# Kernel optimization log

Hardware: AMD Instinct MI355X
Metric: run time of the kernel (lower is better)

Reference implementation:

```python
import jax, jax.numpy as jnp
import numpy as np

N_NODES = 50000
N_EDGES = 800000
D = 96        # node_dim
DE = 96       # edge_dim
K_HOPS = 4
K = 2         # module's k; uses edge_attr[:, k-1]


def setup_inputs() -> dict:
    key = jax.random.key(0)
    ks = jax.random.split(key, 12)
    s = 1.0 / np.sqrt(D)
    se = 1.0 / np.sqrt(DE)
    s2 = 1.0 / np.sqrt(2 * D)
    return {
        "V": jax.random.normal(ks[0], (N_NODES, D), jnp.float32),
        "V_in": jax.random.normal(ks[1], (N_NODES, D), jnp.float32),
        "E": jax.random.normal(ks[2], (N_EDGES, DE), jnp.float32),
        "edge_attr": jax.random.uniform(ks[3], (N_EDGES, K_HOPS), jnp.float32),
        "src": jax.random.randint(ks[4], (N_EDGES,), 0, N_NODES),
        "dst": jax.random.randint(ks[5], (N_EDGES,), 0, N_NODES),
        # NodePooling linear A: node_dim -> node_dim
        "A_w": jax.random.uniform(ks[6], (D, D), jnp.float32, -s, s),
        "A_b": jax.random.uniform(ks[7], (D,), jnp.float32, -s, s),
        # M: edge_dim -> node_dim
        "M_w": jax.random.uniform(ks[8], (DE, D), jnp.float32, -se, se),
        "M_b": jax.random.uniform(ks[9], (D,), jnp.float32, -se, se),
        # W: 2*node_dim -> node_dim
        "W_w": jax.random.uniform(ks[10], (2 * D, D), jnp.float32, -s2, s2),
        "W_b": jax.random.uniform(ks[11], (D,), jnp.float32, -s2, s2),
    }


def reference(V, V_in, E, edge_attr, src, dst, A_w, A_b, M_w, M_b, W_w, W_b):
    # V = LeakyReLU(V, 0.2)
    V = jax.nn.leaky_relu(V, negative_slope=0.2)
    # NodePooling: ReLU(Linear(V))
    Vp = jax.nn.relu(V @ A_w + A_b)                      # [N, D]
    # edge projection
    Ep = E @ M_w + M_b                                   # [M, D]
    khop = edge_attr[:, K - 1:K]                         # [M, 1]
    # message: (src['V'] + data['E']) * KHOP, then sum-aggregate to dst
    msg = (Vp[src] + Ep) * khop                          # [M, D]
    agg = jax.ops.segment_sum(msg, dst, num_segments=N_NODES)  # [N, D]
    # cat aggregate with V_in, project, relu
    out = jax.nn.relu(jnp.concatenate([agg, V_in], axis=-1) @ W_w + W_b)
    return out
```

## Files before the change

### kernel.cpp

```cpp
#include <hip/hip_runtime.h>
#include <hip/hip_bf16.h>

#define NN 50000
#define NE 800000
#define DD 96
#define SVP 100
#define CAP 64

typedef float f4 __attribute__((ext_vector_type(4)));
typedef int   i4 __attribute__((ext_vector_type(4)));

__global__ __launch_bounds__(256) void k_vp(
    const float* __restrict__ V, const float* __restrict__ Aw,
    const float* __restrict__ Ab, float* __restrict__ Vp,
    int* __restrict__ cnt)
{
    __shared__ float sW[DD * DD];
    __shared__ float sV[64 * SVP];
    __shared__ float sB[DD];

    const int tid = threadIdx.x;
    const int gt = blockIdx.x * 256 + tid;
    if (gt < NN) cnt[gt] = 0;

    for (int i = tid; i < DD * DD / 4; i += 256)
        reinterpret_cast<f4*>(sW)[i] = reinterpret_cast<const f4*>(Aw)[i];
    if (tid < DD / 4)
        reinterpret_cast<f4*>(sB)[tid] = reinterpret_cast<const f4*>(Ab)[tid];

    const int row0 = blockIdx.x * 64;
    const int nr = min(64, NN - row0);
    for (int i = tid; i < nr * (DD / 4); i += 256) {
        const int r = i / (DD / 4);
        const int c = i % (DD / 4);
        f4 v = reinterpret_cast<const f4*>(V + (size_t)(row0 + r) * DD)[c];
        v[0] = v[0] > 0.f ? v[0] : 0.2f * v[0];
        v[1] = v[1] > 0.f ? v[1] : 0.2f * v[1];
        v[2] = v[2] > 0.f ? v[2] : 0.2f * v[2];
        v[3] = v[3] > 0.f ? v[3] : 0.2f * v[3];
        reinterpret_cast<f4*>(sV + r * SVP)[c] = v;
    }
    __syncthreads();

    const int cg = tid & 15;
    const int rg = tid >> 4;
    const int c0 = cg * 6;
    const int r0 = rg * 4;

    float acc[4][6];
#pragma unroll
    for (int rr = 0; rr < 4; ++rr)
#pragma unroll
        for (int j = 0; j < 6; ++j) acc[rr][j] = sB[c0 + j];

#pragma unroll 4
    for (int k = 0; k < DD; ++k) {
        float x[4];
#pragma unroll
        for (int rr = 0; rr < 4; ++rr) x[rr] = sV[(r0 + rr) * SVP + k];
#pragma unroll
        for (int j = 0; j < 6; ++j) {
            const float w = sW[k * DD + c0 + j];
#pragma unroll
            for (int rr = 0; rr < 4; ++rr)
                acc[rr][j] = fmaf(x[rr], w, acc[rr][j]);
        }
    }

#pragma unroll
    for (int rr = 0; rr < 4; ++rr) {
        const int row = row0 + r0 + rr;
        if (row < NN) {
#pragma unroll
            for (int j = 0; j < 6; ++j)
                Vp[(size_t)row * DD + c0 + j] = fmaxf(acc[rr][j], 0.f);
        }
    }
}

__global__ __launch_bounds__(256) void k_scatter(
    const int* __restrict__ src, const int* __restrict__ dst,
    const float* __restrict__ ea, int* __restrict__ cnt,
    i4* __restrict__ aux)
{
    const int e = blockIdx.x * 256 + threadIdx.x;
    if (e >= NE) return;
    const int d = dst[e];
    const int pos = atomicAdd(&cnt[d], 1);
    i4 a;
    a.x = src[e];
    a.y = e;
    a.z = __float_as_int(ea[(size_t)e * 4 + 1]);
    a.w = 0;
    if (pos < CAP)
        __builtin_nontemporal_store(a, aux + (size_t)d * CAP + pos);
}

__global__ __launch_bounds__(256, 4) void k_aggout(
    const float* __restrict__ Vp, const float* __restrict__ E,
    const int* __restrict__ cnt, const i4* __restrict__ aux,
    const float* __restrict__ Vin, const float* __restrict__ Mw,
    const float* __restrict__ Mb, const float* __restrict__ Ww,
    const float* __restrict__ Wb, float* __restrict__ out)
{
    __shared__ float sAgg[32 * SVP];
    __shared__ float sG[32 * SVP];
    __shared__ float sW[32 * DD];
    __shared__ float sB[DD];
    __shared__ float sS[32];

    const int tid = threadIdx.x;
    const int row0 = blockIdx.x * 32;

    {
        const int grp = tid >> 5;
        const int gl = tid & 31;
        const bool act = (gl < 24);

        i4 apre[4];
        int n[4];
#pragma unroll
        for (int i = 0; i < 4; ++i) {
            const int node = row0 + grp * 4 + i;
            const bool ok = (node < NN);
            apre[i] = ok ? __builtin_nontemporal_load(aux + (size_t)node * CAP + gl)
                         : i4{0, 0, 0, 0};
            n[i] = ok ? min(cnt[node], CAP) : 0;
        }

#pragma unroll
        for (int i = 0; i < 4; ++i) {
            const int nl = grp * 4 + i;
            const int node = row0 + nl;
            if (node >= NN) break;

            f4 av = {0.f, 0.f, 0.f, 0.f};
            f4 ag = {0.f, 0.f, 0.f, 0.f};
            float wsum = 0.f;

            i4 a = apre[i];
            const int nfirst = min(n[i], 32);

            int j = 0;
            for (; j + 8 <= nfirst; j += 8) {
                int ss[8], ee[8];
                float ww[8];
#pragma unroll
                for (int q = 0; q < 8; ++q) {
                    ss[q] = __shfl(a.x, j + q, 32);
                    ee[q] = __shfl(a.y, j + q, 32);
                    ww[q] = __shfl(__int_as_float(a.z), j + q, 32);
                }
                f4 Ev[8], Vv[8];
#pragma unroll
                for (int q = 0; q < 8; ++q) {
                    if (act) {
                        Ev[q] = __builtin_nontemporal_load(
                            reinterpret_cast<const f4*>(E + (size_t)ee[q] * DD) + gl);
                        Vv[q] = *(reinterpret_cast<const f4*>(Vp + (size_t)ss[q] * DD) + gl);
                    } else {
                        Ev[q] = f4{0, 0, 0, 0};
                        Vv[q] = f4{0, 0, 0, 0};
                    }
                }
#pragma unroll
                for (int q = 0; q < 8; ++q) {
#pragma unroll
                    for (int c = 0; c < 4; ++c) {
                        av[c] = fmaf(ww[q], Vv[q][c], av[c]);
                        ag[c] = fmaf(ww[q], Ev[q][c], ag[c]);
                    }
                    wsum += ww[q];
                }
            }
            for (; j + 4 <= nfirst; j += 4) {
                int ss[4], ee[4];
                float ww[4];
#pragma unroll
                for (int q = 0; q < 4; ++q) {
                    ss[q] = __shfl(a.x, j + q, 32);
                    ee[q] = __shfl(a.y, j + q, 32);
                    ww[q] = __shfl(__int_as_float(a.z), j + q, 32);
                }
                f4 Ev[4], Vv[4];
#pragma unroll
                for (int q = 0; q < 4; ++q) {
                    if (act) {
                        Ev[q] = __builtin_nontemporal_load(
                            reinterpret_cast<const f4*>(E + (size_t)ee[q] * DD) + gl);
                        Vv[q] = *(reinterpret_cast<const f4*>(Vp + (size_t)ss[q] * DD) + gl);
                    } else {
                        Ev[q] = f4{0, 0, 0, 0};
                        Vv[q] = f4{0, 0, 0, 0};
                    }
                }
#pragma unroll
                for (int q = 0; q < 4; ++q) {
#pragma unroll
                    for (int c = 0; c < 4; ++c) {
                        av[c] = fmaf(ww[q], Vv[q][c], av[c]);
                        ag[c] = fmaf(ww[q], Ev[q][c], ag[c]);
                    }
                    wsum += ww[q];
                }
            }
            for (; j < nfirst; ++j) {
                const int s0 = __shfl(a.x, j, 32), e0 = __shfl(a.y, j, 32);
                const float w0 = __shfl(__int_as_float(a.z), j, 32);
                f4 E0 = {0, 0, 0, 0}, V0 = {0, 0, 0, 0};
                if (act) {
                    E0 = __builtin_nontemporal_load(
                        reinterpret_cast<const f4*>(E + (size_t)e0 * DD) + gl);
                    V0 = *(reinterpret_cast<const f4*>(Vp + (size_t)s0 * DD) + gl);
                }
#pragma unroll
                for (int c = 0; c < 4; ++c) {
                    av[c] = fmaf(w0, V0[c], av[c]);
                    ag[c] = fmaf(w0, E0[c], ag[c]);
                }
                wsum += w0;
            }

            if (n[i] > 32) {
                i4 a2 = __builtin_nontemporal_load(
                    aux + (size_t)node * CAP + 32 + gl);
                const int rem = n[i] - 32;
                for (int jj = 0; jj < rem; ++jj) {
                    const int s0 = __shfl(a2.x, jj, 32), e0 = __shfl(a2.y, jj, 32);
                    const float w0 = __shfl(__int_as_float(a2.z), jj, 32);
                    f4 E0 = {0, 0, 0, 0}, V0 = {0, 0, 0, 0};
                    if (act) {
                        E0 = __builtin_nontemporal_load(
                            reinterpret_cast<const f4*>(E + (size_t)e0 * DD) + gl);
                        V0 = *(reinterpret_cast<const f4*>(Vp + (size_t)s0 * DD) + gl);
                    }
#pragma unroll
                    for (int c = 0; c < 4; ++c) {
                        av[c] = fmaf(w0, V0[c], av[c]);
                        ag[c] = fmaf(w0, E0[c], ag[c]);
                    }
                    wsum += w0;
                }
            }

            if (act) {
                *reinterpret_cast<f4*>(sAgg + nl * SVP + gl * 4) = av;
                *reinterpret_cast<f4*>(sG + nl * SVP + gl * 4) = ag;
            }
            if (gl == 0) sS[nl] = wsum;
        }
    }
    __syncthreads();

    const int cg = tid & 15;
    const int rg = tid >> 4;
    const int c0 = cg * 6;
    const int r0 = rg * 2;

    auto loadW = [&](const float* wsrc) {
        for (int i = tid; i < 32 * DD / 4; i += 256)
            reinterpret_cast<f4*>(sW)[i] = reinterpret_cast<const f4*>(wsrc)[i];
    };
    auto loadB = [&](const float* bsrc) {
        if (tid < DD / 4)
            reinterpret_cast<f4*>(sB)[tid] = reinterpret_cast<const f4*>(bsrc)[tid];
    };

    loadW(Mw); loadB(Mb);
    __syncthreads();

    float a[2][6];
#pragma unroll
    for (int rr = 0; rr < 2; ++rr) {
        const float sv = sS[r0 + rr];
#pragma unroll
        for (int j = 0; j < 6; ++j)
            a[rr][j] = sAgg[(r0 + rr) * SVP + c0 + j] + sv * sB[c0 + j];
    }
#pragma unroll
    for (int ch = 0; ch < 3; ++ch) {
        if (ch) {
            __syncthreads();
            loadW(Mw + ch * 32 * DD);
            __syncthreads();
        }
        const int kb = ch * 32;
#pragma unroll 4
        for (int k = 0; k < 32; ++k) {
            const float x0 = sG[r0 * SVP + kb + k];
            const float x1 = sG[(r0 + 1) * SVP + kb + k];
#pragma unroll
            for (int j = 0; j < 6; ++j) {
                const float w = sW[k * DD + c0 + j];
                a[0][j] = fmaf(x0, w, a[0][j]);
                a[1][j] = fmaf(x1, w, a[1][j]);
            }
        }
    }
    __syncthreads();
#pragma unroll
    for (int rr = 0; rr < 2; ++rr)
#pragma unroll
        for (int j = 0; j < 6; ++j)
            sAgg[(r0 + rr) * SVP + c0 + j] = a[rr][j];

    {
        const int nr = min(32, NN - row0);
        __syncthreads();
        for (int i = tid; i < nr * (DD / 4); i += 256) {
            const int r = i / (DD / 4);
            const int c = i % (DD / 4);
            reinterpret_cast<f4*>(sG + r * SVP)[c] =
                reinterpret_cast<const f4*>(Vin + (size_t)(row0 + r) * DD)[c];
        }
    }

    loadW(Ww); loadB(Wb);
    __syncthreads();

    float o[2][6];
#pragma unroll
    for (int rr = 0; rr < 2; ++rr)
#pragma unroll
        for (int j = 0; j < 6; ++j) o[rr][j] = sB[c0 + j];
#pragma unroll
    for (int ch = 0; ch < 3; ++ch) {
        if (ch) {
            __syncthreads();
            loadW(Ww + ch * 32 * DD);
            __syncthreads();
        }
        const int kb = ch * 32;
#pragma unroll 4
        for (int k = 0; k < 32; ++k) {
            const float x0 = sAgg[r0 * SVP + kb + k];
            const float x1 = sAgg[(r0 + 1) * SVP + kb + k];
#pragma unroll
            for (int j = 0; j < 6; ++j) {
                const float w = sW[k * DD + c0 + j];
                o[0][j] = fmaf(x0, w, o[0][j]);
                o[1][j] = fmaf(x1, w, o[1][j]);
            }
        }
    }

#pragma unroll
    for (int ch = 0; ch < 3; ++ch) {
        __syncthreads();
        loadW(Ww + (size_t)(96 + ch * 32) * DD);
        __syncthreads();
        const int kb = ch * 32;
#pragma unroll 4
        for (int k = 0; k < 32; ++k) {
            const float x0 = sG[r0 * SVP + kb + k];
            const float x1 = sG[(r0 + 1) * SVP + kb + k];
#pragma unroll
            for (int j = 0; j < 6; ++j) {
                const float w = sW[k * DD + c0 + j];
                o[0][j] = fmaf(x0, w, o[0][j]);
                o[1][j] = fmaf(x1, w, o[1][j]);
            }
        }
    }

#pragma unroll
    for (int rr = 0; rr < 2; ++rr) {
        const int row = row0 + r0 + rr;
        if (row < NN) {
#pragma unroll
            for (int j = 0; j < 6; ++j)
                out[(size_t)row * DD + c0 + j] = fmaxf(o[rr][j], 0.f);
        }
    }
}

extern "C" void kernel_launch(void* const* d_in, const int* in_sizes, int n_in,
                              void* d_out, int out_size, void* d_ws, size_t ws_size,
                              hipStream_t stream)
{
    const float* V   = (const float*)d_in[0];
    const float* Vin = (const float*)d_in[1];
    const float* E   = (const float*)d_in[2];
    const float* ea  = (const float*)d_in[3];
    const int*   src = (const int*)d_in[4];
    const int*   dst = (const int*)d_in[5];
    const float* Aw  = (const float*)d_in[6];
    const float* Ab  = (const float*)d_in[7];
    const float* Mw  = (const float*)d_in[8];
    const float* Mb  = (const float*)d_in[9];
    const float* Ww  = (const float*)d_in[10];
    const float* Wb  = (const float*)d_in[11];
    float* out = (float*)d_out;

    float* Vp  = (float*)d_ws;
    int*   cnt = (int*)(Vp + (size_t)NN * DD);
    size_t aux_off = (size_t)NN * DD + NN;
    aux_off = (aux_off + 3) & ~(size_t)3;
    i4*    aux = (i4*)((float*)d_ws + aux_off);

    k_vp<<<(NN + 63) / 64, 256, 0, stream>>>(V, Aw, Ab, Vp, cnt);
    k_scatter<<<(NE + 255) / 256, 256, 0, stream>>>(src, dst, ea, cnt, aux);
    k_aggout<<<(NN + 31) / 32, 256, 0, stream>>>(Vp, E, cnt, aux, Vin,
                                                 Mw, Mb, Ww, Wb, out);
}
```

Measured before the change: 226.9 us.

## Pre-stream edge features in scatter kernel to warm cache for aggregation

The scatter kernel now streams the whole E tensor and sums it into a value kept alive by an empty asm, so E lines are pulled into cache before the aggregation kernel gathers them. The E gathers in the aggregation kernel switch from nontemporal to normal loads so they can hit those cached lines. V_in loads and output stores become nontemporal, and the edge_attr read becomes one 16-byte vector load. The cost is a full extra pass over E, which is larger than the last-level cache, so the warmed lines may be evicted before aggregation uses them.

```diff
diff --git a/kernel.cpp b/kernel.cpp
--- a/kernel.cpp
+++ b/kernel.cpp
@@ -81,16 +81,30 @@
 __global__ __launch_bounds__(256) void k_scatter(
     const int* __restrict__ src, const int* __restrict__ dst,
     const float* __restrict__ ea, int* __restrict__ cnt,
-    i4* __restrict__ aux)
+    i4* __restrict__ aux, const float* __restrict__ E)
 {
     const int e = blockIdx.x * 256 + threadIdx.x;
     if (e >= NE) return;
+
+    {
+        const f4* Ef = reinterpret_cast<const f4*>(E);
+        f4 s = {0.f, 0.f, 0.f, 0.f};
+#pragma unroll
+        for (int q = 0; q < 24; ++q) {
+            const f4 t = Ef[(size_t)q * NE + e];
+            s[0] += t[0]; s[1] += t[1]; s[2] += t[2]; s[3] += t[3];
+        }
+        float keep = s[0] + s[1] + s[2] + s[3];
+        asm volatile("" :: "v"(keep));
+    }
+
     const int d = dst[e];
     const int pos = atomicAdd(&cnt[d], 1);
+    const f4 eav = *reinterpret_cast<const f4*>(ea + (size_t)e * 4);
     i4 a;
     a.x = src[e];
     a.y = e;
-    a.z = __float_as_int(ea[(size_t)e * 4 + 1]);
+    a.z = __float_as_int(eav[1]);
     a.w = 0;
     if (pos < CAP)
         __builtin_nontemporal_store(a, aux + (size_t)d * CAP + pos);
@@ -155,8 +169,7 @@
 #pragma unroll
                 for (int q = 0; q < 8; ++q) {
                     if (act) {
-                        Ev[q] = __builtin_nontemporal_load(
-                            reinterpret_cast<const f4*>(E + (size_t)ee[q] * DD) + gl);
+                        Ev[q] = *(reinterpret_cast<const f4*>(E + (size_t)ee[q] * DD) + gl);
                         Vv[q] = *(reinterpret_cast<const f4*>(Vp + (size_t)ss[q] * DD) + gl);
                     } else {
                         Ev[q] = f4{0, 0, 0, 0};
@@ -186,8 +199,7 @@
 #pragma unroll
                 for (int q = 0; q < 4; ++q) {
                     if (act) {
-                        Ev[q] = __builtin_nontemporal_load(
-                            reinterpret_cast<const f4*>(E + (size_t)ee[q] * DD) + gl);
+                        Ev[q] = *(reinterpret_cast<const f4*>(E + (size_t)ee[q] * DD) + gl);
                         Vv[q] = *(reinterpret_cast<const f4*>(Vp + (size_t)ss[q] * DD) + gl);
                     } else {
                         Ev[q] = f4{0, 0, 0, 0};
@@ -209,8 +221,7 @@
                 const float w0 = __shfl(__int_as_float(a.z), j, 32);
                 f4 E0 = {0, 0, 0, 0}, V0 = {0, 0, 0, 0};
                 if (act) {
-                    E0 = __builtin_nontemporal_load(
-                        reinterpret_cast<const f4*>(E + (size_t)e0 * DD) + gl);
+                    E0 = *(reinterpret_cast<const f4*>(E + (size_t)e0 * DD) + gl);
                     V0 = *(reinterpret_cast<const f4*>(Vp + (size_t)s0 * DD) + gl);
                 }
 #pragma unroll
@@ -230,8 +241,7 @@
                     const float w0 = __shfl(__int_as_float(a2.z), jj, 32);
                     f4 E0 = {0, 0, 0, 0}, V0 = {0, 0, 0, 0};
                     if (act) {
-                        E0 = __builtin_nontemporal_load(
-                            reinterpret_cast<const f4*>(E + (size_t)e0 * DD) + gl);
+                        E0 = *(reinterpret_cast<const f4*>(E + (size_t)e0 * DD) + gl);
                         V0 = *(reinterpret_cast<const f4*>(Vp + (size_t)s0 * DD) + gl);
                     }
 #pragma unroll
@@ -310,8 +320,8 @@
         for (int i = tid; i < nr * (DD / 4); i += 256) {
             const int r = i / (DD / 4);
             const int c = i % (DD / 4);
-            reinterpret_cast<f4*>(sG + r * SVP)[c] =
-                reinterpret_cast<const f4*>(Vin + (size_t)(row0 + r) * DD)[c];
+            reinterpret_cast<f4*>(sG + r * SVP)[c] = __builtin_nontemporal_load(
+                reinterpret_cast<const f4*>(Vin + (size_t)(row0 + r) * DD) + c);
         }
     }
 
@@ -367,9 +377,15 @@
     for (int rr = 0; rr < 2; ++rr) {
         const int row = row0 + r0 + rr;
         if (row < NN) {
-#pragma unroll
-            for (int j = 0; j < 6; ++j)
-                out[(size_t)row * DD + c0 + j] = fmaxf(o[rr][j], 0.f);
+            f4 lo = {fmaxf(o[rr][0], 0.f), fmaxf(o[rr][1], 0.f),
+                     fmaxf(o[rr][2], 0.f), fmaxf(o[rr][3], 0.f)};
+            float* op = out + (size_t)row * DD + c0;
+            __builtin_nontemporal_store(lo[0], op + 0);
+            __builtin_nontemporal_store(lo[1], op + 1);
+            __builtin_nontemporal_store(lo[2], op + 2);
+            __builtin_nontemporal_store(lo[3], op + 3);
+            __builtin_nontemporal_store(fmaxf(o[rr][4], 0.f), op + 4);
+            __builtin_nontemporal_store(fmaxf(o[rr][5], 0.f), op + 5);
         }
     }
 }
@@ -399,7 +415,7 @@
     i4*    aux = (i4*)((float*)d_ws + aux_off);
 
     k_vp<<<(NN + 63) / 64, 256, 0, stream>>>(V, Aw, Ab, Vp, cnt);
-    k_scatter<<<(NE + 255) / 256, 256, 0, stream>>>(src, dst, ea, cnt, aux);
+    k_scatter<<<(NE + 255) / 256, 256, 0, stream>>>(src, dst, ea, cnt, aux, E);
     k_aggout<<<(NN + 31) / 32, 256, 0, stream>>>(Vp, E, cnt, aux, Vin,
                                                  Mw, Mb, Ww, Wb, out);
 }
```

Result: slower. 276.5 us (+21.8%).

## Double-buffer E row gathers into LDS via global_load_lds with wave-per-node aggregation

Applied to the files above, without the earlier changes.

Reworks the gather phase so each 64-lane wave handles 8 nodes in turn. Rows of E are streamed into a per-wave double-buffered LDS stage with direct global-to-LDS loads, and the next chunk is prefetched while the current one is accumulated. Vp rows are still read into registers, split across two half-waves whose partial sums are combined with shuffles. This aims to hide gather latency and use all lanes. In exchange it adds waitcnt/sched_barrier hand-tuning, drops the occupancy hint, and processes nodes serially per wave with less memory-level parallelism across nodes.

```diff
diff --git a/kernel.cpp b/kernel.cpp
--- a/kernel.cpp
+++ b/kernel.cpp
@@ -9,6 +9,8 @@
 
 typedef float f4 __attribute__((ext_vector_type(4)));
 typedef int   i4 __attribute__((ext_vector_type(4)));
+typedef const __attribute__((address_space(1))) float gfloat_t;
+typedef __attribute__((address_space(3))) float lfloat_t;
 
 __global__ __launch_bounds__(256) void k_vp(
     const float* __restrict__ V, const float* __restrict__ Aw,
@@ -96,7 +98,7 @@
         __builtin_nontemporal_store(a, aux + (size_t)d * CAP + pos);
 }
 
-__global__ __launch_bounds__(256, 4) void k_aggout(
+__global__ __launch_bounds__(256) void k_aggout(
     const float* __restrict__ Vp, const float* __restrict__ E,
     const int* __restrict__ cnt, const i4* __restrict__ aux,
     const float* __restrict__ Vin, const float* __restrict__ Mw,
@@ -105,153 +107,124 @@
 {
     __shared__ float sAgg[32 * SVP];
     __shared__ float sG[32 * SVP];
-    __shared__ float sW[32 * DD];
+    __shared__ float sStage[4 * 2 * 768];
     __shared__ float sB[DD];
     __shared__ float sS[32];
 
     const int tid = threadIdx.x;
+    const int lane = tid & 63;
+    const int wid = tid >> 6;
     const int row0 = blockIdx.x * 32;
 
     {
-        const int grp = tid >> 5;
-        const int gl = tid & 31;
-        const bool act = (gl < 24);
-
-        i4 apre[4];
-        int n[4];
-#pragma unroll
-        for (int i = 0; i < 4; ++i) {
-            const int node = row0 + grp * 4 + i;
-            const bool ok = (node < NN);
-            apre[i] = ok ? __builtin_nontemporal_load(aux + (size_t)node * CAP + gl)
-                         : i4{0, 0, 0, 0};
-            n[i] = ok ? min(cnt[node], CAP) : 0;
-        }
-
-#pragma unroll
-        for (int i = 0; i < 4; ++i) {
-            const int nl = grp * 4 + i;
+        const int c4l = lane % 24;
+        const int rsel = (lane >= 24 && lane < 48) ? 1 : 0;
+        const int stgwave = wid * 1536;
+
+        for (int i = 0; i < 8; ++i) {
+            const int nl = wid * 8 + i;
             const int node = row0 + nl;
             if (node >= NN) break;
 
+            const i4 a = __builtin_nontemporal_load(aux + (size_t)node * CAP + lane);
+            const int n = min(cnt[node], CAP);
+
+            if (n == 0) {
+                if (lane < 24) {
+                    f4 z = {0.f, 0.f, 0.f, 0.f};
+                    *reinterpret_cast<f4*>(sAgg + nl * SVP + lane * 4) = z;
+                    *reinterpret_cast<f4*>(sG + nl * SVP + lane * 4) = z;
+                }
+                if (lane == 0) sS[nl] = 0.f;
+                continue;
+            }
+
+            const int nm1 = n - 1;
+            const float wz = __int_as_float(a.z);
+            const int nsc = (n + 7) >> 3;
+
             f4 av = {0.f, 0.f, 0.f, 0.f};
             f4 ag = {0.f, 0.f, 0.f, 0.f};
-            float wsum = 0.f;
-
-            i4 a = apre[i];
-            const int nfirst = min(n[i], 32);
-
-            int j = 0;
-            for (; j + 8 <= nfirst; j += 8) {
-                int ss[8], ee[8];
-                float ww[8];
-#pragma unroll
-                for (int q = 0; q < 8; ++q) {
-                    ss[q] = __shfl(a.x, j + q, 32);
-                    ee[q] = __shfl(a.y, j + q, 32);
-                    ww[q] = __shfl(__int_as_float(a.z), j + q, 32);
-                }
-                f4 Ev[8], Vv[8];
-#pragma unroll
-                for (int q = 0; q < 8; ++q) {
-                    if (act) {
-                        Ev[q] = __builtin_nontemporal_load(
-                            reinterpret_cast<const f4*>(E + (size_t)ee[q] * DD) + gl);
-                        Vv[q] = *(reinterpret_cast<const f4*>(Vp + (size_t)ss[q] * DD) + gl);
-                    } else {
-                        Ev[q] = f4{0, 0, 0, 0};
-                        Vv[q] = f4{0, 0, 0, 0};
+
+            auto STAGE = [&](int sc, int b) {
+                const int base = stgwave + b * 768;
+#pragma unroll
+                for (int k = 0; k < 3; ++k) {
+                    const int m = k * 64 + lane;
+                    const int row = m / 24;
+                    const int col = m - row * 24;
+                    const int gr = min(sc * 8 + row, nm1);
+                    const int eid = __shfl(a.y, gr, 64);
+                    __builtin_amdgcn_global_load_lds(
+                        (gfloat_t*)(E + (size_t)eid * DD + col * 4),
+                        (lfloat_t*)(sStage + base + k * 256),
+                        16, 0, 0);
+                }
+            };
+
+            STAGE(0, 0);
+
+            for (int sc = 0; sc < nsc; ++sc) {
+                f4 Vv[4];
+                float wr[4];
+#pragma unroll
+                for (int q = 0; q < 4; ++q) {
+                    const int r = sc * 8 + q * 2 + rsel;
+                    const int rc = min(r, nm1);
+                    const int sid = __shfl(a.x, rc, 64);
+                    const float w = __shfl(wz, rc, 64);
+                    wr[q] = (r < n) ? w : 0.f;
+                    Vv[q] = *(reinterpret_cast<const f4*>(Vp + (size_t)sid * DD) + c4l);
+                }
+
+                if (sc + 1 < nsc) {
+                    STAGE(sc + 1, (sc + 1) & 1);
+                    asm volatile("s_waitcnt vmcnt(3)" ::: "memory");
+                } else {
+                    asm volatile("s_waitcnt vmcnt(0)" ::: "memory");
+                }
+                __builtin_amdgcn_sched_barrier(0);
+
+                const float* stg = sStage + stgwave + (sc & 1) * 768;
+#pragma unroll
+                for (int q = 0; q < 4; ++q) {
+                    const int rl = q * 2 + rsel;
+                    const f4 Ev = *reinterpret_cast<const f4*>(stg + rl * 96 + c4l * 4);
+#pragma unroll
+                    for (int c = 0; c < 4; ++c) {
+                        av[c] = fmaf(wr[q], Vv[q][c], av[c]);
+                        ag[c] = fmaf(wr[q], Ev[c], ag[c]);
                     }
                 }
-#pragma unroll
-                for (int q = 0; q < 8; ++q) {
-#pragma unroll
-                    for (int c = 0; c < 4; ++c) {
-                        av[c] = fmaf(ww[q], Vv[q][c], av[c]);
-                        ag[c] = fmaf(ww[q], Ev[q][c], ag[c]);
-                    }
-                    wsum += ww[q];
-                }
-            }
-            for (; j + 4 <= nfirst; j += 4) {
-                int ss[4], ee[4];
-                float ww[4];
-#pragma unroll
-                for (int q = 0; q < 4; ++q) {
-                    ss[q] = __shfl(a.x, j + q, 32);
-                    ee[q] = __shfl(a.y, j + q, 32);
-                    ww[q] = __shfl(__int_as_float(a.z), j + q, 32);
-                }
-                f4 Ev[4], Vv[4];
-#pragma unroll
-                for (int q = 0; q < 4; ++q) {
-                    if (act) {
-                        Ev[q] = __builtin_nontemporal_load(
-                            reinterpret_cast<const f4*>(E + (size_t)ee[q] * DD) + gl);
-                        Vv[q] = *(reinterpret_cast<const f4*>(Vp + (size_t)ss[q] * DD) + gl);
-                    } else {
-                        Ev[q] = f4{0, 0, 0, 0};
-                        Vv[q] = f4{0, 0, 0, 0};
-                    }
-                }
-#pragma unroll
-                for (int q = 0; q < 4; ++q) {
-#pragma unroll
-                    for (int c = 0; c < 4; ++c) {
-                        av[c] = fmaf(ww[q], Vv[q][c], av[c]);
-                        ag[c] = fmaf(ww[q], Ev[q][c], ag[c]);
-                    }
-                    wsum += ww[q];
-                }
-            }
-            for (; j < nfirst; ++j) {
-                const int s0 = __shfl(a.x, j, 32), e0 = __shfl(a.y, j, 32);
-                const float w0 = __shfl(__int_as_float(a.z), j, 32);
-                f4 E0 = {0, 0, 0, 0}, V0 = {0, 0, 0, 0};
-                if (act) {
-                    E0 = __builtin_nontemporal_load(
-                        reinterpret_cast<const f4*>(E + (size_t)e0 * DD) + gl);
-                    V0 = *(reinterpret_cast<const f4*>(Vp + (size_t)s0 * DD) + gl);
-                }
+            }
+
+            float wl = (lane < n) ? wz : 0.f;
+#pragma unroll
+            for (int d = 1; d < 64; d <<= 1)
+                wl += __shfl_xor(wl, d, 64);
+
+            f4 av2, ag2;
+#pragma unroll
+            for (int c = 0; c < 4; ++c) {
+                av2[c] = __shfl(av[c], (lane & 31) + 24, 64);
+                ag2[c] = __shfl(ag[c], (lane & 31) + 24, 64);
+            }
+            if (lane < 24) {
+                f4 avt, agt;
 #pragma unroll
                 for (int c = 0; c < 4; ++c) {
-                    av[c] = fmaf(w0, V0[c], av[c]);
-                    ag[c] = fmaf(w0, E0[c], ag[c]);
-                }
-                wsum += w0;
-            }
-
-            if (n[i] > 32) {
-                i4 a2 = __builtin_nontemporal_load(
-                    aux + (size_t)node * CAP + 32 + gl);
-                const int rem = n[i] - 32;
-                for (int jj = 0; jj < rem; ++jj) {
-                    const int s0 = __shfl(a2.x, jj, 32), e0 = __shfl(a2.y, jj, 32);
-                    const float w0 = __shfl(__int_as_float(a2.z), jj, 32);
-                    f4 E0 = {0, 0, 0, 0}, V0 = {0, 0, 0, 0};
-                    if (act) {
-                        E0 = __builtin_nontemporal_load(
-                            reinterpret_cast<const f4*>(E + (size_t)e0 * DD) + gl);
-                        V0 = *(reinterpret_cast<const f4*>(Vp + (size_t)s0 * DD) + gl);
-                    }
-#pragma unroll
-                    for (int c = 0; c < 4; ++c) {
-                        av[c] = fmaf(w0, V0[c], av[c]);
-                        ag[c] = fmaf(w0, E0[c], ag[c]);
-                    }
-                    wsum += w0;
-                }
-            }
-
-            if (act) {
-                *reinterpret_cast<f4*>(sAgg + nl * SVP + gl * 4) = av;
-                *reinterpret_cast<f4*>(sG + nl * SVP + gl * 4) = ag;
-            }
-            if (gl == 0) sS[nl] = wsum;
-        }
-    }
-    __syncthreads();
-
+                    avt[c] = av[c] + av2[c];
+                    agt[c] = ag[c] + ag2[c];
+                }
+                *reinterpret_cast<f4*>(sAgg + nl * SVP + lane * 4) = avt;
+                *reinterpret_cast<f4*>(sG + nl * SVP + lane * 4) = agt;
+            }
+            if (lane == 0) sS[nl] = wl;
+        }
+    }
+    __syncthreads();
+
+    float* const sW = sStage;
     const int cg = tid & 15;
     const int rg = tid >> 4;
     const int c0 = cg * 6;
```

After: 270.9 us. 19.4% more time.
